# Performance work log

Hardware: AMD Instinct MI355X
Metric: run time of the kernel (lower is better)

The kernel has to match this reference:

```python
import jax, jax.numpy as jnp
import numpy as np
from jax import lax

B, C_IN, H, W = 64, 64, 36, 36
N_UNITS = 2048


def setup_inputs() -> dict:
    key = jax.random.key(0)
    k1, k2, k3, k4 = jax.random.split(key, 4)
    x = jax.random.normal(k1, (B, C_IN, H, W), dtype=jnp.float32)
    feat_weights = jax.random.normal(k2, (N_UNITS, C_IN, 1, 1), dtype=jnp.float32) * 0.1
    biases = jax.random.normal(k3, (N_UNITS,), dtype=jnp.float32)
    space_weights = jax.random.normal(k4, (N_UNITS, H, W), dtype=jnp.float32) * 0.05
    return {"x": x, "feat_weights": feat_weights, "biases": biases,
            "space_weights": space_weights}


def reference(x, feat_weights, biases, space_weights):
    # 1x1 channel-mixing conv: [B,Cin,H,W] x [U,Cin] -> [B,U,H,W]
    feat = jnp.einsum('bchw,uc->buhw', x, feat_weights[:, :, 0, 0])
    # grouped (depthwise, groups=n_units) valid conv; kernel spans full spatial
    # extent, so output is [B, U, 1, 1]
    space = lax.conv_general_dilated(
        feat, space_weights[:, None, :, :],
        window_strides=(1, 1), padding='VALID',
        feature_group_count=N_UNITS,
        dimension_numbers=('NCHW', 'OIHW', 'NCHW'))
    out = space + biases[None, :, None, None]
    return out
```

## Files before the change

kernel.cpp:

```cpp
#include <hip/hip_runtime.h>
#include <hip/hip_bf16.h>
#include <stdint.h>

#define NB 64
#define NC 64
#define NU 2048
#define K_REAL 1296
#define K_PAD  1344
#define M_ROWS 4096

#define BM 256
#define BN 128

typedef __attribute__((ext_vector_type(4))) float f32x4;
typedef __attribute__((ext_vector_type(8))) short bf16x8;

__device__ __forceinline__ unsigned short f2bf_rne(float f) {
  union { float f; uint32_t u; } v; v.f = f;
  uint32_t u = v.u;
  return (unsigned short)((u + 0x7FFFu + ((u >> 16) & 1u)) >> 16);
}

__global__ void convert_pad_kernel(const float* __restrict__ x,
                                   const float* __restrict__ sw,
                                   unsigned short* __restrict__ dst) {
  const int KB = K_PAD / 8;
  const int total = (M_ROWS + NU) * KB;
  for (int idx = blockIdx.x * blockDim.x + threadIdx.x; idx < total;
       idx += gridDim.x * blockDim.x) {
    int r  = idx / KB;
    int kb = idx - r * KB;
    int k0 = kb * 8;
    uint32_t p0 = 0, p1 = 0, p2 = 0, p3 = 0;
    if (k0 + 8 <= K_REAL) {
      const float* srow = (r < M_ROWS) ? (x + (size_t)r * K_REAL)
                                       : (sw + (size_t)(r - M_ROWS) * K_REAL);
      const float4* s = (const float4*)(srow + k0);
      float4 f0 = s[0];
      float4 f1 = s[1];
      p0 = (uint32_t)f2bf_rne(f0.x) | ((uint32_t)f2bf_rne(f0.y) << 16);
      p1 = (uint32_t)f2bf_rne(f0.z) | ((uint32_t)f2bf_rne(f0.w) << 16);
      p2 = (uint32_t)f2bf_rne(f1.x) | ((uint32_t)f2bf_rne(f1.y) << 16);
      p3 = (uint32_t)f2bf_rne(f1.z) | ((uint32_t)f2bf_rne(f1.w) << 16);
    }
    uint4 o; o.x = p0; o.y = p1; o.z = p2; o.w = p3;
    *(uint4*)(dst + (size_t)r * K_PAD + k0) = o;
  }
}

__global__ __launch_bounds__(512, 1)
void fused_readout_gemm(const unsigned short* __restrict__ Abf,
                        const unsigned short* __restrict__ Bbf,
                        const float* __restrict__ fw,
                        const float* __restrict__ bias,
                        float* __restrict__ out) {
  __shared__ unsigned short As[2][2][8192];
  __shared__ unsigned short Bs[2][2][4096];

  const int tid  = threadIdx.x;
  const int lane = tid & 63;
  const int w    = tid >> 6;
  const int wm   = w >> 1;
  const int wn   = w & 1;
  const int g    = lane >> 4;
  const int rl   = lane & 15;

  const int braw  = (int)blockIdx.x;
  const int bid   = (braw & 7) * 32 + (braw >> 3);
  const int tileM = bid >> 4;
  const int tileN = bid & 15;
  const int rowA0 = tileM * BM;
  const int colB0 = tileN * BN;

  const int lc  = tid ^ ((tid >> 3) & 3);
  const int sr  = lc >> 2;
  const int sc  = lc & 3;
  const unsigned short* srcA = Abf + (size_t)(rowA0 + sr) * K_PAD + sc * 8;
  const unsigned short* srcB = Bbf + (size_t)(colB0 + sr) * K_PAD + sc * 8;

  const int laneOff = rl * 64 + ((g * 16) ^ (((rl >> 1) & 3) << 4));

#define GLOAD(dst, src)                                                         \
  __builtin_amdgcn_global_load_lds(                                             \
      (const __attribute__((address_space(1))) unsigned int*)(const void*)(src),\
      (__attribute__((address_space(3))) unsigned int*)(void*)(dst), 16, 0, 0)

#define SLOT(buf, s, kk)                                                        \
  do {                                                                          \
    char* _pa = (char*)&As[buf][s][0];                                          \
    GLOAD(_pa + tid * 16, srcA + (kk));                                         \
    GLOAD(_pa + 8192 + tid * 16, srcA + (size_t)128 * K_PAD + (kk));            \
    GLOAD((char*)&Bs[buf][s][0] + tid * 16, srcB + (kk));                       \
  } while (0)

#define LDFRAGS(buf, ks)                                                        \
  do {                                                                          \
    const char* _pa = (const char*)&As[buf][ks][0] + wm * 4096 + laneOff;       \
    av[0] = *(const bf16x8*)(_pa);                                              \
    av[1] = *(const bf16x8*)(_pa + 1024);                                       \
    av[2] = *(const bf16x8*)(_pa + 2048);                                       \
    av[3] = *(const bf16x8*)(_pa + 3072);                                       \
    const char* _pb = (const char*)&Bs[buf][ks][0] + wn * 4096 + laneOff;       \
    bv[0] = *(const bf16x8*)(_pb);                                              \
    bv[1] = *(const bf16x8*)(_pb + 1024);                                       \
    bv[2] = *(const bf16x8*)(_pb + 2048);                                       \
    bv[3] = *(const bf16x8*)(_pb + 3072);                                       \
  } while (0)

#define MFMA16()                                                                \
  do {                                                                          \
    __builtin_amdgcn_s_setprio(1);                                              \
    _Pragma("unroll") for (int _m = 0; _m < 4; ++_m)                            \
      _Pragma("unroll") for (int _n = 0; _n < 4; ++_n)                          \
        acc[_m][_n] = __builtin_amdgcn_mfma_f32_16x16x32_bf16(                  \
            av[_m], bv[_n], acc[_m][_n], 0, 0, 0);                              \
    __builtin_amdgcn_s_setprio(0);                                              \
  } while (0)

#define BAR()                                                                   \
  do { __builtin_amdgcn_s_barrier(); __builtin_amdgcn_sched_barrier(0); } while (0)
#define VMW(N)                                                                  \
  do { asm volatile("s_waitcnt vmcnt(" #N ")" ::: "memory");                    \
       __builtin_amdgcn_sched_barrier(0); } while (0)

  f32x4 acc[4][4];
#pragma unroll
  for (int m = 0; m < 4; ++m)
#pragma unroll
    for (int n = 0; n < 4; ++n) acc[m][n] = (f32x4)0.f;

  bf16x8 av[4], bv[4];

  SLOT(0, 0, 0);
  SLOT(0, 1, 32);
  SLOT(1, 0, 64);
  VMW(6); BAR();

#pragma unroll 1
  for (int it = 0; it < 9; ++it) {
    const int t1 = 2 * it + 1;
    LDFRAGS(0, 0); SLOT(1, 1, t1 * 64 + 32);       BAR(); MFMA16(); VMW(6); BAR();
    LDFRAGS(0, 1); SLOT(0, 0, (t1 + 1) * 64);      BAR(); MFMA16(); VMW(6); BAR();
    LDFRAGS(1, 0); SLOT(0, 1, (t1 + 1) * 64 + 32); BAR(); MFMA16(); VMW(6); BAR();
    LDFRAGS(1, 1); SLOT(1, 0, (t1 + 2) * 64);      BAR(); MFMA16(); VMW(6); BAR();
  }
  LDFRAGS(0, 0); SLOT(1, 1, 19 * 64 + 32); BAR(); MFMA16(); VMW(6); BAR();
  LDFRAGS(0, 1); SLOT(0, 0, 20 * 64);      BAR(); MFMA16(); VMW(6); BAR();
  LDFRAGS(1, 0); SLOT(0, 1, 20 * 64 + 32); BAR(); MFMA16(); VMW(6); BAR();
  LDFRAGS(1, 1);                           BAR(); MFMA16(); VMW(3); BAR();
  LDFRAGS(0, 0);                           BAR(); MFMA16(); VMW(0); BAR();
  LDFRAGS(0, 1);                           BAR(); MFMA16();

#undef GLOAD
#undef SLOT
#undef LDFRAGS
#undef MFMA16
#undef BAR
#undef VMW

  const int bidx = tileM * 4 + wm;
  float vtmp[4];
#pragma unroll
  for (int n = 0; n < 4; ++n) {
    const int u = colB0 + wn * 64 + n * 16 + rl;
    const float* fwrow = fw + (size_t)u * NC;
    float s = 0.f;
#pragma unroll
    for (int m = 0; m < 4; ++m) {
      float4 w4 = *(const float4*)(fwrow + m * 16 + g * 4);
      f32x4 a_ = acc[m][n];
      s += w4.x * a_[0] + w4.y * a_[1] + w4.z * a_[2] + w4.w * a_[3];
    }
    s += __shfl_xor(s, 16, 64);
    s += __shfl_xor(s, 32, 64);
    vtmp[n] = s;
  }
  const int ucol = colB0 + wn * 64 + lane;
  float r = (g == 0) ? vtmp[0] : (g == 1) ? vtmp[1] : (g == 2) ? vtmp[2] : vtmp[3];
  out[(size_t)bidx * NU + ucol] = r + bias[ucol];
}

extern "C" void kernel_launch(void* const* d_in, const int* in_sizes, int n_in,
                              void* d_out, int out_size, void* d_ws, size_t ws_size,
                              hipStream_t stream) {
  const float* x    = (const float*)d_in[0];
  const float* fw   = (const float*)d_in[1];
  const float* bias = (const float*)d_in[2];
  const float* sw   = (const float*)d_in[3];
  float* out = (float*)d_out;

  unsigned short* Abf = (unsigned short*)d_ws;
  unsigned short* Bbf = Abf + (size_t)M_ROWS * K_PAD;

  {
    int total = (M_ROWS + NU) * (K_PAD / 8);
    int blocks = (total + 255) / 256;
    if (blocks > 2048) blocks = 2048;
    convert_pad_kernel<<<blocks, 256, 0, stream>>>(x, sw, Abf);
  }

  fused_readout_gemm<<<dim3(256), 512, 0, stream>>>(Abf, Bbf, fw, bias, out);
}
```

Baseline: 42.61 us.

## Deepen GEMM LDS pipeline to five stages and remap tiles per XCD

Replaces the 4-slot double-buffered K pipeline with a 5-slot ring buffer that keeps three K-slices of global-to-LDS loads in flight instead of two, so more memory latency is hidden behind MFMA work. It also changes the block-to-tile mapping so each XCD handles a 4x8 rectangle of M/N tiles, which should improve L2 reuse of A and B rows within a die. LDS use grows from 96KB to 120KB, which is acceptable at one block per CU but leaves little headroom.

```diff
diff --git a/kernel.cpp b/kernel.cpp
--- a/kernel.cpp
+++ b/kernel.cpp
@@ -11,6 +11,7 @@
 
 #define BM 256
 #define BN 128
+#define NKS 42
 
 typedef __attribute__((ext_vector_type(4))) float f32x4;
 typedef __attribute__((ext_vector_type(8))) short bf16x8;
@@ -54,8 +55,8 @@
                         const float* __restrict__ fw,
                         const float* __restrict__ bias,
                         float* __restrict__ out) {
-  __shared__ unsigned short As[2][2][8192];
-  __shared__ unsigned short Bs[2][2][4096];
+  __shared__ unsigned short As[5][8192];
+  __shared__ unsigned short Bs[5][4096];
 
   const int tid  = threadIdx.x;
   const int lane = tid & 63;
@@ -66,9 +67,10 @@
   const int rl   = lane & 15;
 
   const int braw  = (int)blockIdx.x;
-  const int bid   = (braw & 7) * 32 + (braw >> 3);
-  const int tileM = bid >> 4;
-  const int tileN = bid & 15;
+  const int xcd   = braw & 7;
+  const int idx   = braw >> 3;
+  const int tileM = (xcd >> 1) * 4 + (idx & 3);
+  const int tileN = (xcd & 1) * 8 + (idx >> 2);
   const int rowA0 = tileM * BM;
   const int colB0 = tileN * BN;
 
@@ -85,22 +87,22 @@
       (const __attribute__((address_space(1))) unsigned int*)(const void*)(src),\
       (__attribute__((address_space(3))) unsigned int*)(void*)(dst), 16, 0, 0)
 
-#define SLOT(buf, s, kk)                                                        \
+#define SLOT(j, koff)                                                           \
   do {                                                                          \
-    char* _pa = (char*)&As[buf][s][0];                                          \
-    GLOAD(_pa + tid * 16, srcA + (kk));                                         \
-    GLOAD(_pa + 8192 + tid * 16, srcA + (size_t)128 * K_PAD + (kk));            \
-    GLOAD((char*)&Bs[buf][s][0] + tid * 16, srcB + (kk));                       \
+    char* _pa = (char*)&As[j][0];                                               \
+    GLOAD(_pa + tid * 16, srcA + (koff));                                       \
+    GLOAD(_pa + 8192 + tid * 16, srcA + (size_t)128 * K_PAD + (koff));          \
+    GLOAD((char*)&Bs[j][0] + tid * 16, srcB + (koff));                          \
   } while (0)
 
-#define LDFRAGS(buf, ks)                                                        \
+#define LDFRAGS(j)                                                              \
   do {                                                                          \
-    const char* _pa = (const char*)&As[buf][ks][0] + wm * 4096 + laneOff;       \
+    const char* _pa = (const char*)&As[j][0] + wm * 4096 + laneOff;             \
     av[0] = *(const bf16x8*)(_pa);                                              \
     av[1] = *(const bf16x8*)(_pa + 1024);                                       \
     av[2] = *(const bf16x8*)(_pa + 2048);                                       \
     av[3] = *(const bf16x8*)(_pa + 3072);                                       \
-    const char* _pb = (const char*)&Bs[buf][ks][0] + wn * 4096 + laneOff;       \
+    const char* _pb = (const char*)&Bs[j][0] + wn * 4096 + laneOff;             \
     bv[0] = *(const bf16x8*)(_pb);                                              \
     bv[1] = *(const bf16x8*)(_pb + 1024);                                       \
     bv[2] = *(const bf16x8*)(_pb + 2048);                                       \
@@ -131,25 +133,26 @@
 
   bf16x8 av[4], bv[4];
 
-  SLOT(0, 0, 0);
-  SLOT(0, 1, 32);
-  SLOT(1, 0, 64);
-  VMW(6); BAR();
-
+  SLOT(0, 0); SLOT(1, 32); SLOT(2, 64); SLOT(3, 96);
+  VMW(9); BAR();
+
+  int kb = 128;
 #pragma unroll 1
-  for (int it = 0; it < 9; ++it) {
-    const int t1 = 2 * it + 1;
-    LDFRAGS(0, 0); SLOT(1, 1, t1 * 64 + 32);       BAR(); MFMA16(); VMW(6); BAR();
-    LDFRAGS(0, 1); SLOT(0, 0, (t1 + 1) * 64);      BAR(); MFMA16(); VMW(6); BAR();
-    LDFRAGS(1, 0); SLOT(0, 1, (t1 + 1) * 64 + 32); BAR(); MFMA16(); VMW(6); BAR();
-    LDFRAGS(1, 1); SLOT(1, 0, (t1 + 2) * 64);      BAR(); MFMA16(); VMW(6); BAR();
-  }
-  LDFRAGS(0, 0); SLOT(1, 1, 19 * 64 + 32); BAR(); MFMA16(); VMW(6); BAR();
-  LDFRAGS(0, 1); SLOT(0, 0, 20 * 64);      BAR(); MFMA16(); VMW(6); BAR();
-  LDFRAGS(1, 0); SLOT(0, 1, 20 * 64 + 32); BAR(); MFMA16(); VMW(6); BAR();
-  LDFRAGS(1, 1);                           BAR(); MFMA16(); VMW(3); BAR();
-  LDFRAGS(0, 0);                           BAR(); MFMA16(); VMW(0); BAR();
-  LDFRAGS(0, 1);                           BAR(); MFMA16();
+  for (int it = 0; it < 7; ++it) {
+    LDFRAGS(0); SLOT(4, kb);       BAR(); MFMA16(); VMW(9); BAR();
+    LDFRAGS(1); SLOT(0, kb + 32);  BAR(); MFMA16(); VMW(9); BAR();
+    LDFRAGS(2); SLOT(1, kb + 64);  BAR(); MFMA16(); VMW(9); BAR();
+    LDFRAGS(3); SLOT(2, kb + 96);  BAR(); MFMA16(); VMW(9); BAR();
+    LDFRAGS(4); SLOT(3, kb + 128); BAR(); MFMA16(); VMW(9); BAR();
+    kb += 160;
+  }
+  LDFRAGS(0); SLOT(4, 1248); BAR(); MFMA16(); VMW(9); BAR();
+  LDFRAGS(1); SLOT(0, 1280); BAR(); MFMA16(); VMW(9); BAR();
+  LDFRAGS(2); SLOT(1, 1312); BAR(); MFMA16(); VMW(9); BAR();
+  LDFRAGS(3);                BAR(); MFMA16(); VMW(6); BAR();
+  LDFRAGS(4);                BAR(); MFMA16(); VMW(3); BAR();
+  LDFRAGS(0);                BAR(); MFMA16(); VMW(0); BAR();
+  LDFRAGS(1);                BAR(); MFMA16();
 
 #undef GLOAD
 #undef SLOT
```

New measurement: 42.24 us. About the same (-0.9%).
